# Kernel optimization log

Measured on AMD Instinct MI355X. Metric: run time of the kernel, lower is better.

Reference implementation:

```python
import jax, jax.numpy as jnp
import numpy as np

B, LD, LE = 32, 256, 258          # batch, decoder len (split_num), encoder len (split_num+2)
ENC, DEC, HID = 512, 512, 512     # encoder_size, decoder_size(=GRU hidden), GRU hidden
MLP, NL = 256, 4                  # biaffine mlp size, num transition labels


def setup_inputs() -> dict:
    key = jax.random.key(0)
    ks = jax.random.split(key, 12)
    s = 0.05  # modest init scale for stability
    return {
        "e_outputs": jax.random.normal(ks[0], (B, LE, ENC), jnp.float32),
        "d_inputs": jax.random.normal(ks[1], (B, LD, HID), jnp.float32),
        "h0": jax.random.normal(ks[2], (B, HID), jnp.float32),
        "W_ih": jax.random.normal(ks[3], (3 * HID, HID), jnp.float32) * s,
        "W_hh": jax.random.normal(ks[4], (3 * HID, HID), jnp.float32) * s,
        "b_ih": jnp.zeros((3 * HID,), jnp.float32),
        "b_hh": jnp.zeros((3 * HID,), jnp.float32),
        "e_mlp_w": jax.random.normal(ks[5], (MLP, ENC), jnp.float32) * s,
        "e_mlp_b": jnp.zeros((MLP,), jnp.float32),
        "d_mlp_w": jax.random.normal(ks[6], (MLP, DEC), jnp.float32) * s,
        "d_mlp_b": jnp.zeros((MLP,), jnp.float32),
        "W_e": jax.random.normal(ks[7], (NL, MLP), jnp.float32) * s,
        "W_d": jax.random.normal(ks[8], (NL, MLP), jnp.float32) * s,
        "U": jax.random.normal(ks[9], (NL, MLP, MLP), jnp.float32) * s,
        "b_aff": jnp.zeros((NL, 1, 1), jnp.float32),
    }


def reference(e_outputs, d_inputs, h0, W_ih, W_hh, b_ih, b_hh,
              e_mlp_w, e_mlp_b, d_mlp_w, d_mlp_b, W_e, W_d, U, b_aff):
    def gru_step(h, x):
        gi = x @ W_ih.T + b_ih            # (B, 3H)
        gh = h @ W_hh.T + b_hh            # (B, 3H)
        i_r, i_z, i_n = jnp.split(gi, 3, axis=-1)
        h_r, h_z, h_n = jnp.split(gh, 3, axis=-1)
        r = jax.nn.sigmoid(i_r + h_r)
        z = jax.nn.sigmoid(i_z + h_z)
        n = jnp.tanh(i_n + r * h_n)
        h_new = (1.0 - z) * n + z * h
        return h_new, h_new

    xs = jnp.swapaxes(d_inputs, 0, 1)     # (LD, B, HID)
    _, hs = jax.lax.scan(gru_step, h0, xs)
    d_outputs = jnp.swapaxes(hs, 0, 1)    # (B, LD, HID)

    # --- biaffine pointer scoring (BiAffineAttention.forward) ---
    e_h = jax.nn.relu(e_outputs @ e_mlp_w.T + e_mlp_b)   # (B, LE, MLP)
    d_h = jax.nn.relu(d_outputs @ d_mlp_w.T + d_mlp_b)   # (B, LD, MLP)

    out_e = jnp.einsum('lh,beh->ble', W_e, e_h)[:, :, None, :]   # (B, NL, 1, LE)
    out_d = jnp.einsum('lh,bdh->bld', W_d, d_h)[:, :, :, None]   # (B, NL, LD, 1)
    out_u = jnp.einsum('bdh,lhk,bek->blde', d_h, U, e_h)         # (B, NL, LD, LE)

    out = out_e + out_d + out_u + b_aff                          # b_aff: (NL,1,1)
    return jnp.transpose(out, (0, 2, 3, 1))                      # (B, LD, LE, NL)
```

## Files before the change

kernel.cpp:

```cpp
#include <hip/hip_runtime.h>
#include <hip/hip_fp16.h>
#include <math.h>

#define NB   32
#define LD   256
#define LE   258
#define HID  512
#define H3   1536
#define MLP  256
#define NL   4

typedef _Float16 h2 __attribute__((ext_vector_type(2)));

__device__ __forceinline__ uint32_t load_l2(const uint32_t* p){
  uint32_t v;
  asm volatile("global_load_dword %0, %1, off sc0\n\t"
               "s_waitcnt vmcnt(0)"
               : "=&v"(v) : "v"(p) : "memory");
  return v;
}

__global__ void k_init(uint32_t* __restrict__ hb){
  int i = blockIdx.x*256 + threadIdx.x;
  if (i < 4*NB*HID) hb[i] = 0u;
}

__global__ __launch_bounds__(192,1)
void k_gru(const float* __restrict__ GI, const float* __restrict__ W_hh,
           const float* __restrict__ b_hh, const float* __restrict__ h0,
           float* __restrict__ dout,
           uint32_t* __restrict__ hbufL,
           uint32_t* __restrict__ hbufG){
  const int wg  = blockIdx.x;
  const int b   = wg & 31, g = wg >> 5;
  const int tid = threadIdx.x;
  const int sect = tid >> 6;
  const int u    = tid & 63;
  const int c    = sect*HID + g*64 + u;

  __shared__ __align__(16) float h_lds[HID];
  __shared__ float zs[64], gs[64], ns[64];

  h2 w[256];
  const float4* wr = (const float4*)(W_hh + (size_t)c*HID);
  #pragma unroll
  for (int i=0;i<128;i++){
    float4 v = wr[i];
    h2 p0; p0[0]=(_Float16)v.x; p0[1]=(_Float16)v.y;
    h2 p1; p1[0]=(_Float16)v.z; p1[1]=(_Float16)v.w;
    w[2*i] = p0; w[2*i+1] = p1;
  }
  const float bh = b_hh[c];
  float h_old = (tid < 64) ? h0[(size_t)b*HID + g*64 + u] : 0.f;
  const float* gi_base = GI + (size_t)b*LD*H3 + c;
  float* db = dout + (size_t)b*LD*HID + g*64;

  const int w0 = tid, w1 = tid + 192, w2 = tid + 384;

  for (int i=tid;i<HID;i+=192) h_lds[i] = h0[(size_t)b*HID + i];
  __syncthreads();

  float gi = gi_base[0];
  for (int t=0;t<LD;t++){
    float a0=0.f, a1=0.f, a2=0.f, a3=0.f;
    const float4* hl = (const float4*)h_lds;
    #pragma unroll
    for (int kk=0;kk<128;kk++){
      float4 hv = hl[kk];
      h2 q0 = w[2*kk], q1 = w[2*kk+1];
      a0 = fmaf((float)q0[0], hv.x, a0);
      a1 = fmaf((float)q0[1], hv.y, a1);
      a2 = fmaf((float)q1[0], hv.z, a2);
      a3 = fmaf((float)q1[1], hv.w, a3);
    }
    float hh = (a0+a1) + (a2+a3) + bh;
    if (sect==1)      zs[u] = gi + hh;
    else if (sect==2){ gs[u] = gi; ns[u] = hh; }
    float pre_r = gi + hh;
    __syncthreads();

    if (t < LD-1){
      uint32_t* hbL = hbufL + (size_t)((t+1)&1)*(NB*HID) + (size_t)b*HID;
      uint32_t* hbG = hbufG + (size_t)((t+1)&1)*(NB*HID) + (size_t)b*HID;
      const uint32_t want = (uint32_t)(t+1) & 0xFFu;
      if (tid < 64){
        float r = __builtin_amdgcn_rcpf(1.f + __expf(-pre_r));
        float z = __builtin_amdgcn_rcpf(1.f + __expf(-zs[u]));
        float x = gs[u] + r*ns[u];
        float e2 = __expf(2.f*x);
        float n = 1.f - 2.f*__builtin_amdgcn_rcpf(e2 + 1.f);
        float hnew = (1.f-z)*n + z*h_old;
        h_old = hnew;
        uint32_t wb = (__builtin_bit_cast(uint32_t, hnew) & ~0xFFu) | want;
        *(volatile uint32_t*)(hbL + g*64 + u) = wb;
        __hip_atomic_store(hbG + g*64 + u, wb,
                           __ATOMIC_RELAXED, __HIP_MEMORY_SCOPE_AGENT);
        db[(size_t)t*HID + u] = hnew;
      }
      float gnext = gi_base[(size_t)(t+1)*H3];
      uint32_t* hlu = (uint32_t*)h_lds;
      bool n0 = true, n1 = true, n2 = (w2 < HID);
      int it = 0;
      while ((n0 | n1 | n2) && it < (1<<20)){
        const bool useG = ((it & 3) == 3);
        if (n0){
          uint32_t x = useG ? __hip_atomic_load(hbG+w0, __ATOMIC_RELAXED, __HIP_MEMORY_SCOPE_AGENT)
                            : load_l2(hbL+w0);
          if ((x & 0xFFu) == want){ hlu[w0] = x; n0 = false; }
        }
        if (n1){
          uint32_t x = useG ? __hip_atomic_load(hbG+w1, __ATOMIC_RELAXED, __HIP_MEMORY_SCOPE_AGENT)
                            : load_l2(hbL+w1);
          if ((x & 0xFFu) == want){ hlu[w1] = x; n1 = false; }
        }
        if (n2){
          uint32_t x = useG ? __hip_atomic_load(hbG+w2, __ATOMIC_RELAXED, __HIP_MEMORY_SCOPE_AGENT)
                            : load_l2(hbL+w2);
          if ((x & 0xFFu) == want){ hlu[w2] = x; n2 = false; }
        }
        ++it;
      }
      __syncthreads();
      gi = gnext;
    } else {
      if (tid < 64){
        float r = __builtin_amdgcn_rcpf(1.f + __expf(-pre_r));
        float z = __builtin_amdgcn_rcpf(1.f + __expf(-zs[u]));
        float x = gs[u] + r*ns[u];
        float e2 = __expf(2.f*x);
        float n = 1.f - 2.f*__builtin_amdgcn_rcpf(e2 + 1.f);
        float hnew = (1.f-z)*n + z*h_old;
        db[(size_t)t*HID + u] = hnew;
      }
    }
  }
}

template<int BIAS, int RELU>
__global__ __launch_bounds__(256)
void k_gemm_nt(const float* __restrict__ A, const float* __restrict__ Bm,
               const float* __restrict__ bias, float* __restrict__ C,
               int M, int N, int K){
  __shared__ float As[32][68];
  __shared__ float Bs[32][68];
  const int bm = blockIdx.y*64, bn = blockIdx.x*64;
  const int tid = threadIdx.x;
  const int tx = tid & 15, ty = tid >> 4;
  const int lr = tid >> 3;
  const int lk = (tid & 7) << 2;
  const float* A0 = A + (size_t)(bm+lr)*K + lk;
  const float* A1 = A + (size_t)(bm+lr+32)*K + lk;
  const float* B0 = Bm + (size_t)(bn+lr)*K + lk;
  const float* B1 = Bm + (size_t)(bn+lr+32)*K + lk;
  float acc[4][4] = {};
  for (int k0=0;k0<K;k0+=32){
    float4 a0 = *(const float4*)(A0 + k0);
    float4 a1 = *(const float4*)(A1 + k0);
    float4 b0 = *(const float4*)(B0 + k0);
    float4 b1 = *(const float4*)(B1 + k0);
    __syncthreads();
    As[lk+0][lr]=a0.x; As[lk+1][lr]=a0.y; As[lk+2][lr]=a0.z; As[lk+3][lr]=a0.w;
    As[lk+0][lr+32]=a1.x; As[lk+1][lr+32]=a1.y; As[lk+2][lr+32]=a1.z; As[lk+3][lr+32]=a1.w;
    Bs[lk+0][lr]=b0.x; Bs[lk+1][lr]=b0.y; Bs[lk+2][lr]=b0.z; Bs[lk+3][lr]=b0.w;
    Bs[lk+0][lr+32]=b1.x; Bs[lk+1][lr+32]=b1.y; Bs[lk+2][lr+32]=b1.z; Bs[lk+3][lr+32]=b1.w;
    __syncthreads();
    #pragma unroll
    for (int kk=0;kk<32;kk++){
      float4 av = *(const float4*)&As[kk][ty<<2];
      float4 bv = *(const float4*)&Bs[kk][tx<<2];
      float a4[4] = {av.x,av.y,av.z,av.w};
      float b4[4] = {bv.x,bv.y,bv.z,bv.w};
      #pragma unroll
      for (int i=0;i<4;i++)
        #pragma unroll
        for (int j=0;j<4;j++)
          acc[i][j] = fmaf(a4[i], b4[j], acc[i][j]);
    }
  }
  #pragma unroll
  for (int i=0;i<4;i++){
    int m = bm + (ty<<2) + i;
    #pragma unroll
    for (int j=0;j<4;j++){
      int n = bn + (tx<<2) + j;
      float v = acc[i][j];
      if (BIAS) v += bias[n];
      if (RELU) v = fmaxf(v, 0.f);
      C[(size_t)m*N + n] = v;
    }
  }
}

__global__ __launch_bounds__(256)
void k_gemm_nn_T(const float* __restrict__ A, const float* __restrict__ U,
                 float* __restrict__ T){
  __shared__ float As[32][68];
  __shared__ float Bs[32][68];
  const int l = blockIdx.z;
  const float* Bm = U + (size_t)l*MLP*MLP;
  float* C = T + (size_t)l*NB*LD*MLP;
  const int bm = blockIdx.y*64, bn = blockIdx.x*64;
  const int tid = threadIdx.x;
  const int tx = tid & 15, ty = tid >> 4;
  const int lr = tid >> 3;
  const int lk = (tid & 7) << 2;
  const int bk_r = tid >> 4;
  const int bn_c = (tid & 15) << 2;
  const float* A0 = A + (size_t)(bm+lr)*MLP + lk;
  const float* A1 = A + (size_t)(bm+lr+32)*MLP + lk;
  float acc[4][4] = {};
  for (int k0=0;k0<MLP;k0+=32){
    float4 a0 = *(const float4*)(A0 + k0);
    float4 a1 = *(const float4*)(A1 + k0);
    float4 u0 = *(const float4*)(Bm + (size_t)(k0+bk_r)*MLP + bn + bn_c);
    float4 u1 = *(const float4*)(Bm + (size_t)(k0+bk_r+16)*MLP + bn + bn_c);
    __syncthreads();
    As[lk+0][lr]=a0.x; As[lk+1][lr]=a0.y; As[lk+2][lr]=a0.z; As[lk+3][lr]=a0.w;
    As[lk+0][lr+32]=a1.x; As[lk+1][lr+32]=a1.y; As[lk+2][lr+32]=a1.z; As[lk+3][lr+32]=a1.w;
    *(float4*)&Bs[bk_r][bn_c]    = u0;
    *(float4*)&Bs[bk_r+16][bn_c] = u1;
    __syncthreads();
    #pragma unroll
    for (int kk=0;kk<32;kk++){
      float4 av = *(const float4*)&As[kk][ty<<2];
      float4 bv = *(const float4*)&Bs[kk][tx<<2];
      float a4[4] = {av.x,av.y,av.z,av.w};
      float b4[4] = {bv.x,bv.y,bv.z,bv.w};
      #pragma unroll
      for (int i=0;i<4;i++)
        #pragma unroll
        for (int j=0;j<4;j++)
          acc[i][j] = fmaf(a4[i], b4[j], acc[i][j]);
    }
  }
  #pragma unroll
  for (int i=0;i<4;i++){
    int m = bm + (ty<<2) + i;
    #pragma unroll
    for (int j=0;j<4;j++)
      C[(size_t)m*MLP + bn + (tx<<2) + j] = acc[i][j];
  }
}

__global__ void k_bilinear(const float* __restrict__ W, const float* __restrict__ Hm,
                           float* __restrict__ S, int Lrows){
  int idx = blockIdx.x*256 + threadIdx.x;
  if (idx >= NB*Lrows) return;
  int b = idx / Lrows, r = idx - b*Lrows;
  const float* row = Hm + (size_t)idx*MLP;
  float acc[NL] = {0.f,0.f,0.f,0.f};
  for (int h=0; h<MLP; h+=4){
    float4 x = *(const float4*)(row + h);
    #pragma unroll
    for (int l=0;l<NL;l++){
      float4 w = *(const float4*)(W + l*MLP + h);
      acc[l] += x.x*w.x + x.y*w.y + x.z*w.z + x.w*w.w;
    }
  }
  #pragma unroll
  for (int l=0;l<NL;l++) S[((size_t)b*NL + l)*Lrows + r] = acc[l];
}

__global__ __launch_bounds__(256)
void k_s2(const float* __restrict__ T, const float* __restrict__ eh,
          const float* __restrict__ sd, const float* __restrict__ se,
          const float* __restrict__ baff, float* __restrict__ out){
  __shared__ float As[32][68];
  __shared__ float Bs[32][68];
  const int b = blockIdx.z;
  const int d0 = blockIdx.y*64, e0 = blockIdx.x*64;
  const int tid = threadIdx.x;
  const int tx = tid & 15, ty = tid >> 4;
  const int lr = tid >> 3;
  const int lk = (tid & 7) << 2;
  const float* EH = eh + (size_t)b*LE*MLP;
  for (int l=0;l<NL;l++){
    const float* A = T + ((size_t)(l*NB + b))*LD*MLP;
    float acc[4][4] = {};
    for (int k0=0;k0<MLP;k0+=32){
      float4 a0 = *(const float4*)(A + (size_t)(d0+lr)*MLP + k0 + lk);
      float4 a1 = *(const float4*)(A + (size_t)(d0+lr+32)*MLP + k0 + lk);
      float4 z4 = make_float4(0.f,0.f,0.f,0.f);
      int er0 = e0+lr, er1 = e0+lr+32;
      float4 b0 = (er0<LE) ? *(const float4*)(EH + (size_t)er0*MLP + k0 + lk) : z4;
      float4 b1 = (er1<LE) ? *(const float4*)(EH + (size_t)er1*MLP + k0 + lk) : z4;
      __syncthreads();
      As[lk+0][lr]=a0.x; As[lk+1][lr]=a0.y; As[lk+2][lr]=a0.z; As[lk+3][lr]=a0.w;
      As[lk+0][lr+32]=a1.x; As[lk+1][lr+32]=a1.y; As[lk+2][lr+32]=a1.z; As[lk+3][lr+32]=a1.w;
      Bs[lk+0][lr]=b0.x; Bs[lk+1][lr]=b0.y; Bs[lk+2][lr]=b0.z; Bs[lk+3][lr]=b0.w;
      Bs[lk+0][lr+32]=b1.x; Bs[lk+1][lr+32]=b1.y; Bs[lk+2][lr+32]=b1.z; Bs[lk+3][lr+32]=b1.w;
      __syncthreads();
      #pragma unroll
      for (int kk=0;kk<32;kk++){
        float4 av = *(const float4*)&As[kk][ty<<2];
        float4 bv = *(const float4*)&Bs[kk][tx<<2];
        float a4[4] = {av.x,av.y,av.z,av.w};
        float b4[4] = {bv.x,bv.y,bv.z,bv.w};
        #pragma unroll
        for (int i=0;i<4;i++)
          #pragma unroll
          for (int j=0;j<4;j++)
            acc[i][j] = fmaf(a4[i], b4[j], acc[i][j]);
      }
    }
    float bl = baff[l];
    float sdl[4], sel[4];
    #pragma unroll
    for (int i=0;i<4;i++) sdl[i] = sd[((size_t)b*NL + l)*LD + d0 + (ty<<2) + i];
    #pragma unroll
    for (int j=0;j<4;j++){
      int e = e0 + (tx<<2) + j;
      sel[j] = (e<LE) ? se[((size_t)b*NL + l)*LE + e] : 0.f;
    }
    #pragma unroll
    for (int i=0;i<4;i++){
      int d = d0 + (ty<<2) + i;
      #pragma unroll
      for (int j=0;j<4;j++){
        int e = e0 + (tx<<2) + j;
        if (e < LE)
          out[(((size_t)b*LD + d)*LE + e)*NL + l] = acc[i][j] + sdl[i] + sel[j] + bl;
      }
    }
  }
}

extern "C" void kernel_launch(void* const* d_in, const int* in_sizes, int n_in,
                              void* d_out, int out_size, void* d_ws, size_t ws_size,
                              hipStream_t stream){
  const float* e_outputs = (const float*)d_in[0];
  const float* d_inputs  = (const float*)d_in[1];
  const float* h0        = (const float*)d_in[2];
  const float* W_ih      = (const float*)d_in[3];
  const float* W_hh      = (const float*)d_in[4];
  const float* b_ih      = (const float*)d_in[5];
  const float* b_hh      = (const float*)d_in[6];
  const float* e_mlp_w   = (const float*)d_in[7];
  const float* e_mlp_b   = (const float*)d_in[8];
  const float* d_mlp_w   = (const float*)d_in[9];
  const float* d_mlp_b   = (const float*)d_in[10];
  const float* W_e       = (const float*)d_in[11];
  const float* W_d       = (const float*)d_in[12];
  const float* U         = (const float*)d_in[13];
  const float* b_aff     = (const float*)d_in[14];
  float* out = (float*)d_out;
  float* ws  = (float*)d_ws;

  float* GI   = ws;
  float* T    = ws;
  uint32_t* hbufL = (uint32_t*)(ws + 12582912);
  uint32_t* hbufG = hbufL + 2*NB*HID;
  float* dout = ws   + 12582912 + 786432;
  float* eh   = dout + 4194304;
  float* dh   = eh   + 2113536;
  float* se   = dh   + 2097152;
  float* sd   = se   + 33024;

  k_init<<<dim3((4*NB*HID+255)/256), 256, 0, stream>>>(hbufL);
  k_gemm_nt<1,0><<<dim3(H3/64, (NB*LD)/64), 256, 0, stream>>>(d_inputs, W_ih, b_ih, GI, NB*LD, H3, HID);
  k_gemm_nt<1,1><<<dim3(MLP/64, (NB*LE)/64), 256, 0, stream>>>(e_outputs, e_mlp_w, e_mlp_b, eh, NB*LE, MLP, HID);
  k_gru<<<dim3(NB*8), 192, 0, stream>>>(GI, W_hh, b_hh, h0, dout, hbufL, hbufG);
  k_gemm_nt<1,1><<<dim3(MLP/64, (NB*LD)/64), 256, 0, stream>>>(dout, d_mlp_w, d_mlp_b, dh, NB*LD, MLP, HID);
  k_gemm_nn_T<<<dim3(MLP/64, (NB*LD)/64, NL), 256, 0, stream>>>(dh, U, T);
  k_bilinear<<<dim3((NB*LE+255)/256), 256, 0, stream>>>(W_e, eh, se, LE);
  k_bilinear<<<dim3((NB*LD+255)/256), 256, 0, stream>>>(W_d, dh, sd, LD);
  k_s2<<<dim3(5, LD/64, NB), 256, 0, stream>>>(T, eh, sd, se, b_aff, out);
}
```

Baseline: 2.739 ms.

## Simplify GRU cross-workgroup polling, remap batch groups, add 128x128 GEMM tiles

The GRU recurrence drops the dual local/global hidden-state buffers and the inline-asm sc0 loads. It now uses one buffer with agent-scope atomic loads and stores, and adds an s_sleep backoff while polling. Workgroup mapping changes so the 8 workgroups of one batch row are adjacent (b = wg>>3), which changes which CUs or XCDs share a row. A new 128x128-tile fp32 GEMM with 8x8 register blocking replaces the 64x64 kernel for the input-gate and decoder-MLP projections, trading occupancy for more reuse. The sleep may add latency to each of the 255 serial sync steps, and the mapping change may route polling traffic across XCDs differently.

```diff
diff --git a/kernel.cpp b/kernel.cpp
--- a/kernel.cpp
+++ b/kernel.cpp
@@ -12,27 +12,18 @@
 
 typedef _Float16 h2 __attribute__((ext_vector_type(2)));
 
-__device__ __forceinline__ uint32_t load_l2(const uint32_t* p){
-  uint32_t v;
-  asm volatile("global_load_dword %0, %1, off sc0\n\t"
-               "s_waitcnt vmcnt(0)"
-               : "=&v"(v) : "v"(p) : "memory");
-  return v;
-}
-
 __global__ void k_init(uint32_t* __restrict__ hb){
   int i = blockIdx.x*256 + threadIdx.x;
-  if (i < 4*NB*HID) hb[i] = 0u;
+  if (i < 2*NB*HID) hb[i] = 0u;
 }
 
 __global__ __launch_bounds__(192,1)
 void k_gru(const float* __restrict__ GI, const float* __restrict__ W_hh,
            const float* __restrict__ b_hh, const float* __restrict__ h0,
            float* __restrict__ dout,
-           uint32_t* __restrict__ hbufL,
-           uint32_t* __restrict__ hbufG){
+           uint32_t* __restrict__ hbuf){
   const int wg  = blockIdx.x;
-  const int b   = wg & 31, g = wg >> 5;
+  const int b   = wg >> 3, g = wg & 7;
   const int tid = threadIdx.x;
   const int sect = tid >> 6;
   const int u    = tid & 63;
@@ -80,8 +71,7 @@
     __syncthreads();
 
     if (t < LD-1){
-      uint32_t* hbL = hbufL + (size_t)((t+1)&1)*(NB*HID) + (size_t)b*HID;
-      uint32_t* hbG = hbufG + (size_t)((t+1)&1)*(NB*HID) + (size_t)b*HID;
+      uint32_t* hb = hbuf + (size_t)((t+1)&1)*(NB*HID) + (size_t)b*HID;
       const uint32_t want = (uint32_t)(t+1) & 0xFFu;
       if (tid < 64){
         float r = __builtin_amdgcn_rcpf(1.f + __expf(-pre_r));
@@ -92,8 +82,7 @@
         float hnew = (1.f-z)*n + z*h_old;
         h_old = hnew;
         uint32_t wb = (__builtin_bit_cast(uint32_t, hnew) & ~0xFFu) | want;
-        *(volatile uint32_t*)(hbL + g*64 + u) = wb;
-        __hip_atomic_store(hbG + g*64 + u, wb,
+        __hip_atomic_store(hb + g*64 + u, wb,
                            __ATOMIC_RELAXED, __HIP_MEMORY_SCOPE_AGENT);
         db[(size_t)t*HID + u] = hnew;
       }
@@ -102,23 +91,19 @@
       bool n0 = true, n1 = true, n2 = (w2 < HID);
       int it = 0;
       while ((n0 | n1 | n2) && it < (1<<20)){
-        const bool useG = ((it & 3) == 3);
         if (n0){
-          uint32_t x = useG ? __hip_atomic_load(hbG+w0, __ATOMIC_RELAXED, __HIP_MEMORY_SCOPE_AGENT)
-                            : load_l2(hbL+w0);
+          uint32_t x = __hip_atomic_load(hb+w0, __ATOMIC_RELAXED, __HIP_MEMORY_SCOPE_AGENT);
           if ((x & 0xFFu) == want){ hlu[w0] = x; n0 = false; }
         }
         if (n1){
-          uint32_t x = useG ? __hip_atomic_load(hbG+w1, __ATOMIC_RELAXED, __HIP_MEMORY_SCOPE_AGENT)
-                            : load_l2(hbL+w1);
+          uint32_t x = __hip_atomic_load(hb+w1, __ATOMIC_RELAXED, __HIP_MEMORY_SCOPE_AGENT);
           if ((x & 0xFFu) == want){ hlu[w1] = x; n1 = false; }
         }
         if (n2){
-          uint32_t x = useG ? __hip_atomic_load(hbG+w2, __ATOMIC_RELAXED, __HIP_MEMORY_SCOPE_AGENT)
-                            : load_l2(hbL+w2);
+          uint32_t x = __hip_atomic_load(hb+w2, __ATOMIC_RELAXED, __HIP_MEMORY_SCOPE_AGENT);
           if ((x & 0xFFu) == want){ hlu[w2] = x; n2 = false; }
         }
-        ++it;
+        if (n0 | n1 | n2){ ++it; __builtin_amdgcn_s_sleep(1); }
       }
       __syncthreads();
       gi = gnext;
@@ -132,6 +117,61 @@
         float hnew = (1.f-z)*n + z*h_old;
         db[(size_t)t*HID + u] = hnew;
       }
+    }
+  }
+}
+
+template<int BIAS, int RELU>
+__global__ __launch_bounds__(256)
+void k_gemm_nt128(const float* __restrict__ A, const float* __restrict__ Bm,
+                  const float* __restrict__ bias, float* __restrict__ C,
+                  int M, int N, int K){
+  __shared__ float As[16][132];
+  __shared__ float Bs[16][132];
+  const int bm = blockIdx.y*128, bn = blockIdx.x*128;
+  const int tid = threadIdx.x;
+  const int tx = tid & 15, ty = tid >> 4;
+  const int lr = tid >> 1;
+  const int lc = (tid & 1) << 3;
+  const float* Ap = A + (size_t)(bm+lr)*K + lc;
+  const float* Bp = Bm + (size_t)(bn+lr)*K + lc;
+  float acc[8][8] = {};
+  for (int k0=0;k0<K;k0+=16){
+    float4 a0 = *(const float4*)(Ap + k0);
+    float4 a1 = *(const float4*)(Ap + k0 + 4);
+    float4 b0 = *(const float4*)(Bp + k0);
+    float4 b1 = *(const float4*)(Bp + k0 + 4);
+    __syncthreads();
+    As[lc+0][lr]=a0.x; As[lc+1][lr]=a0.y; As[lc+2][lr]=a0.z; As[lc+3][lr]=a0.w;
+    As[lc+4][lr]=a1.x; As[lc+5][lr]=a1.y; As[lc+6][lr]=a1.z; As[lc+7][lr]=a1.w;
+    Bs[lc+0][lr]=b0.x; Bs[lc+1][lr]=b0.y; Bs[lc+2][lr]=b0.z; Bs[lc+3][lr]=b0.w;
+    Bs[lc+4][lr]=b1.x; Bs[lc+5][lr]=b1.y; Bs[lc+6][lr]=b1.z; Bs[lc+7][lr]=b1.w;
+    __syncthreads();
+    #pragma unroll
+    for (int kk=0;kk<16;kk++){
+      float4 va0 = *(const float4*)&As[kk][ty<<3];
+      float4 va1 = *(const float4*)&As[kk][(ty<<3)+4];
+      float4 vb0 = *(const float4*)&Bs[kk][tx<<3];
+      float4 vb1 = *(const float4*)&Bs[kk][(tx<<3)+4];
+      float a8[8] = {va0.x,va0.y,va0.z,va0.w,va1.x,va1.y,va1.z,va1.w};
+      float b8[8] = {vb0.x,vb0.y,vb0.z,vb0.w,vb1.x,vb1.y,vb1.z,vb1.w};
+      #pragma unroll
+      for (int i=0;i<8;i++)
+        #pragma unroll
+        for (int j=0;j<8;j++)
+          acc[i][j] = fmaf(a8[i], b8[j], acc[i][j]);
+    }
+  }
+  #pragma unroll
+  for (int i=0;i<8;i++){
+    int m = bm + (ty<<3) + i;
+    #pragma unroll
+    for (int j=0;j<8;j++){
+      int n = bn + (tx<<3) + j;
+      float v = acc[i][j];
+      if (BIAS) v += bias[n];
+      if (RELU) v = fmaxf(v, 0.f);
+      C[(size_t)m*N + n] = v;
     }
   }
 }
@@ -348,19 +388,18 @@
 
   float* GI   = ws;
   float* T    = ws;
-  uint32_t* hbufL = (uint32_t*)(ws + 12582912);
-  uint32_t* hbufG = hbufL + 2*NB*HID;
+  uint32_t* hbuf = (uint32_t*)(ws + 12582912);
   float* dout = ws   + 12582912 + 786432;
   float* eh   = dout + 4194304;
   float* dh   = eh   + 2113536;
   float* se   = dh   + 2097152;
   float* sd   = se   + 33024;
 
-  k_init<<<dim3((4*NB*HID+255)/256), 256, 0, stream>>>(hbufL);
-  k_gemm_nt<1,0><<<dim3(H3/64, (NB*LD)/64), 256, 0, stream>>>(d_inputs, W_ih, b_ih, GI, NB*LD, H3, HID);
+  k_init<<<dim3((2*NB*HID+255)/256), 256, 0, stream>>>(hbuf);
+  k_gemm_nt128<1,0><<<dim3(H3/128, (NB*LD)/128), 256, 0, stream>>>(d_inputs, W_ih, b_ih, GI, NB*LD, H3, HID);
   k_gemm_nt<1,1><<<dim3(MLP/64, (NB*LE)/64), 256, 0, stream>>>(e_outputs, e_mlp_w, e_mlp_b, eh, NB*LE, MLP, HID);
-  k_gru<<<dim3(NB*8), 192, 0, stream>>>(GI, W_hh, b_hh, h0, dout, hbufL, hbufG);
-  k_gemm_nt<1,1><<<dim3(MLP/64, (NB*LD)/64), 256, 0, stream>>>(dout, d_mlp_w, d_mlp_b, dh, NB*LD, MLP, HID);
+  k_gru<<<dim3(NB*8), 192, 0, stream>>>(GI, W_hh, b_hh, h0, dout, hbuf);
+  k_gemm_nt128<1,1><<<dim3(MLP/128, (NB*LD)/128), 256, 0, stream>>>(dout, d_mlp_w, d_mlp_b, dh, NB*LD, MLP, HID);
   k_gemm_nn_T<<<dim3(MLP/64, (NB*LD)/64, NL), 256, 0, stream>>>(dh, U, T);
   k_bilinear<<<dim3((NB*LE+255)/256), 256, 0, stream>>>(W_e, eh, se, LE);
   k_bilinear<<<dim3((NB*LD+255)/256), 256, 0, stream>>>(W_d, dh, sd, LD);
```

New measurement: 2.559 ms. 6.6% less time.
